# Kernel tuning notes

Hardware: AMD Instinct MI355X
Metric: run time of the kernel (lower is better)

## Reference

```python
import jax, jax.numpy as jnp
import numpy as np

GRAVITY = 9.81007  # pypose default, gravity vector [0,0,g]

# Quaternions are xyzw (pypose SO3 convention). q1*q2 composes rotations R1@R2.

def qmul(q1, q2):
    v1, w1 = q1[..., :3], q1[..., 3:]
    v2, w2 = q2[..., :3], q2[..., 3:]
    w = w1 * w2 - jnp.sum(v1 * v2, axis=-1, keepdims=True)
    v = w1 * v2 + w2 * v1 + jnp.cross(v1, v2)
    return jnp.concatenate([v, w], axis=-1)

def qinv(q):
    return jnp.concatenate([-q[..., :3], q[..., 3:]], axis=-1)

def qrot(q, v):
    # rotate vector v by unit quaternion q: v + 2*cross(qv, cross(qv,v) + qw*v)
    qv, qw = q[..., :3], q[..., 3:]
    t = jnp.cross(qv, v) + qw * v
    return v + 2.0 * jnp.cross(qv, t)

def so3_exp(phi):
    # so3 -> SO3 quaternion: q = [phi*sin(|phi|/2)/|phi|, cos(|phi|/2)]
    theta = jnp.linalg.norm(phi, axis=-1, keepdims=True)
    small = theta < 1e-6
    safe = jnp.where(small, 1.0, theta)
    k = jnp.where(small, 0.5 - theta * theta / 48.0, jnp.sin(0.5 * theta) / safe)
    return jnp.concatenate([phi * k, jnp.cos(0.5 * theta)], axis=-1)


def setup_inputs() -> dict:
    key = jax.random.key(0)
    ks = jax.random.split(key, 7)
    B, F = 64, 32768
    dt = jax.random.uniform(ks[0], (B, F, 1), jnp.float32) * 0.01 + 0.004
    gyro = jax.random.normal(ks[1], (B, F, 3), jnp.float32) * 0.1
    acc = jax.random.normal(ks[2], (B, F, 3), jnp.float32)

    def rand_quat(k, shape):
        q = jax.random.normal(k, shape + (4,), jnp.float32)
        return q / jnp.linalg.norm(q, axis=-1, keepdims=True)

    gt_rot = rand_quat(ks[3], (B, F))      # ground-truth orientations (xyzw)
    init_rot = rand_quat(ks[4], (B, 1))
    init_vel = jax.random.normal(ks[5], (B, 1, 3), jnp.float32)
    init_pos = jax.random.normal(ks[6], (B, 1, 3), jnp.float32)
    return dict(dt=dt, gyro=gyro, acc=acc, gt_rot=gt_rot,
                init_rot=init_rot, init_vel=init_vel, init_pos=init_pos)


def reference(dt, gyro, acc, gt_rot, init_rot, init_vel, init_pos):
    # IMU preintegration (pypose IMUPreintegrator, reset=True, prop_cov=False,
    # training branch: gravity removed in body frame via ground-truth rot).
    g = jnp.array([0.0, 0.0, GRAVITY], dtype=dt.dtype)
    dr = so3_exp(gyro * dt)                                   # (B,F,4) per-step rotation
    # cumulative rotation increment: incre_r[i] = dr_0 * dr_1 * ... * dr_i
    incre_r = jax.lax.associative_scan(qmul, dr, axis=1)      # (B,F,4)
    # gravity-compensated body-frame acceleration
    a = acc - qrot(qinv(gt_rot), g)                           # (B,F,3)
    ra = qrot(incre_r, a)                                     # rotated into init frame
    incre_v = jnp.cumsum(ra * dt, axis=1)                     # (B,F,3)
    v_prev = jnp.concatenate([jnp.zeros_like(incre_v[:, :1]), incre_v[:, :-1]], axis=1)
    incre_p = jnp.cumsum(v_prev * dt + 0.5 * ra * dt * dt, axis=1)
    incre_t = jnp.cumsum(dt, axis=1)                          # (B,F,1)
    # compose with initial state
    rot = qmul(init_rot, incre_r)                             # (B,F,4)
    vel = init_vel + qrot(init_rot, incre_v)                  # (B,F,3)
    pos = init_pos + init_vel * incre_t + qrot(init_rot, incre_p)  # (B,F,3)
    return rot, vel, pos
```

## Files before the change

kernel.cpp:

```cpp
#include <hip/hip_runtime.h>
#include <math.h>

namespace {

constexpr int BLK   = 256;
constexpr int SEQ   = 4;
constexpr int CHUNK = BLK * SEQ;
constexpr int NWAVE = BLK / 64;

struct V3 { float x, y, z; };
struct Q4 { float x, y, z, w; };
struct St { Q4 q; V3 s; V3 p; float T; float pad; };

__device__ __forceinline__ Q4 qmul(const Q4 a, const Q4 b) {
  Q4 r;
  r.x = a.w*b.x + b.w*a.x + a.y*b.z - a.z*b.y;
  r.y = a.w*b.y + b.w*a.y + a.z*b.x - a.x*b.z;
  r.z = a.w*b.z + b.w*a.z + a.x*b.y - a.y*b.x;
  r.w = a.w*b.w - a.x*b.x - a.y*b.y - a.z*b.z;
  return r;
}

__device__ __forceinline__ V3 qrot(const Q4 q, const V3 v) {
  float tx = q.y*v.z - q.z*v.y + q.w*v.x;
  float ty = q.z*v.x - q.x*v.z + q.w*v.y;
  float tz = q.x*v.y - q.y*v.x + q.w*v.z;
  V3 r;
  r.x = v.x + 2.0f*(q.y*tz - q.z*ty);
  r.y = v.y + 2.0f*(q.z*tx - q.x*tz);
  r.z = v.z + 2.0f*(q.x*ty - q.y*tx);
  return r;
}

__device__ __forceinline__ St combine(const St a, const St b) {
  St r;
  r.q = qmul(a.q, b.q);
  V3 rs = qrot(a.q, b.s);
  r.s.x = a.s.x + rs.x;
  r.s.y = a.s.y + rs.y;
  r.s.z = a.s.z + rs.z;
  V3 rp = qrot(a.q, b.p);
  r.p.x = a.p.x + a.s.x*b.T + rp.x;
  r.p.y = a.p.y + a.s.y*b.T + rp.y;
  r.p.z = a.p.z + a.s.z*b.T + rp.z;
  r.T = a.T + b.T;
  r.pad = 0.0f;
  return r;
}

__device__ __forceinline__ St identity_st() {
  St r;
  r.q = {0.0f, 0.0f, 0.0f, 1.0f};
  r.s = {0.0f, 0.0f, 0.0f};
  r.p = {0.0f, 0.0f, 0.0f};
  r.T = 0.0f; r.pad = 0.0f;
  return r;
}

__device__ __forceinline__ St elem_state(float dt, V3 w, V3 ac, Q4 gt) {
  float px = w.x*dt, py = w.y*dt, pz = w.z*dt;
  float t2 = px*px + py*py + pz*pz;
  float k  = 0.5f + t2*(-1.0f/48.0f  + t2*(1.0f/3840.0f));
  float cw = 1.0f + t2*(-0.125f      + t2*(1.0f/384.0f));
  Q4 dr = { px*k, py*k, pz*k, cw };
  Q4 gi = { -gt.x, -gt.y, -gt.z, gt.w };
  V3 g  = { 0.0f, 0.0f, 9.81007f };
  V3 gr = qrot(gi, g);
  V3 a  = { ac.x - gr.x, ac.y - gr.y, ac.z - gr.z };
  V3 ra = qrot(dr, a);
  St e;
  e.q = dr;
  e.s.x = ra.x*dt; e.s.y = ra.y*dt; e.s.z = ra.z*dt;
  float h = 0.5f*dt;
  e.p.x = e.s.x*h; e.p.y = e.s.y*h; e.p.z = e.s.z*h;
  e.T = dt; e.pad = 0.0f;
  return e;
}

__device__ __forceinline__ St shfl_up_st(const St& v, int d) {
  St r;
  r.q.x = __shfl_up(v.q.x, d); r.q.y = __shfl_up(v.q.y, d);
  r.q.z = __shfl_up(v.q.z, d); r.q.w = __shfl_up(v.q.w, d);
  r.s.x = __shfl_up(v.s.x, d); r.s.y = __shfl_up(v.s.y, d);
  r.s.z = __shfl_up(v.s.z, d);
  r.p.x = __shfl_up(v.p.x, d); r.p.y = __shfl_up(v.p.y, d);
  r.p.z = __shfl_up(v.p.z, d);
  r.T   = __shfl_up(v.T, d);   r.pad = 0.0f;
  return r;
}

__device__ __forceinline__ St shfl_down_st(const St& v, int d) {
  St r;
  r.q.x = __shfl_down(v.q.x, d); r.q.y = __shfl_down(v.q.y, d);
  r.q.z = __shfl_down(v.q.z, d); r.q.w = __shfl_down(v.q.w, d);
  r.s.x = __shfl_down(v.s.x, d); r.s.y = __shfl_down(v.s.y, d);
  r.s.z = __shfl_down(v.s.z, d);
  r.p.x = __shfl_down(v.p.x, d); r.p.y = __shfl_down(v.p.y, d);
  r.p.z = __shfl_down(v.p.z, d);
  r.T   = __shfl_down(v.T, d);   r.pad = 0.0f;
  return r;
}

#define BUILD_ELEMS(E)                                                         \
  St E[SEQ];                                                                   \
  {                                                                            \
    float dtv[SEQ]; float gy[SEQ*3]; float acv[SEQ*3]; float gq[SEQ*4];        \
    *((float4*)dtv) = *(const float4*)(dtp + gi);                              \
    _Pragma("unroll")                                                          \
    for (int j = 0; j < 3; ++j) ((float4*)gy)[j]  = ((const float4*)(gyp + gi*3))[j]; \
    _Pragma("unroll")                                                          \
    for (int j = 0; j < 3; ++j) ((float4*)acv)[j] = ((const float4*)(acp + gi*3))[j]; \
    _Pragma("unroll")                                                          \
    for (int j = 0; j < 4; ++j) ((float4*)gq)[j]  = ((const float4*)(gtp + gi*4))[j]; \
    _Pragma("unroll")                                                          \
    for (int i = 0; i < SEQ; ++i)                                              \
      E[i] = elem_state(dtv[i],                                                \
                 {gy[3*i], gy[3*i+1], gy[3*i+2]},                              \
                 {acv[3*i], acv[3*i+1], acv[3*i+2]},                           \
                 {gq[4*i], gq[4*i+1], gq[4*i+2], gq[4*i+3]});                  \
  }

__global__ __launch_bounds__(BLK) void k_agg(
    const float* __restrict__ dtp, const float* __restrict__ gyp,
    const float* __restrict__ acp, const float* __restrict__ gtp,
    St* __restrict__ aggs, int F, int cpb)
{
  const int blk = blockIdx.x;
  const int b = blk / cpb, c = blk - b*cpb;
  const int tid = threadIdx.x;
  const int lane = tid & 63, wv = tid >> 6;
  const size_t gi = (size_t)b*F + (size_t)c*CHUNK + (size_t)tid*SEQ;

  BUILD_ELEMS(e);
  St run = e[0];
  #pragma unroll
  for (int i = 1; i < SEQ; ++i) run = combine(run, e[i]);

  #pragma unroll
  for (int d = 1; d < 64; d <<= 1) run = combine(run, shfl_down_st(run, d));

  __shared__ St sh[NWAVE];
  if (lane == 0) sh[wv] = run;
  __syncthreads();
  if (tid == 0) {
    St t = sh[0];
    #pragma unroll
    for (int k = 1; k < NWAVE; ++k) t = combine(t, sh[k]);
    aggs[blk] = t;
  }
}

__global__ __launch_bounds__(BLK) void k_emit(
    const float* __restrict__ dtp, const float* __restrict__ gyp,
    const float* __restrict__ acp, const float* __restrict__ gtp,
    const St* __restrict__ aggs,
    const float* __restrict__ irp,
    const float* __restrict__ ivp, const float* __restrict__ ipp,
    float* __restrict__ out, int F, int cpb, int B)
{
  const int blk = blockIdx.x;
  const int b = blk / cpb, c = blk - b*cpb;
  const int tid = threadIdx.x;
  const int lane = tid & 63, wv = tid >> 6;
  const size_t gi = (size_t)b*F + (size_t)c*CHUNK + (size_t)tid*SEQ;

  __shared__ St chunkPrefSh;
  __shared__ St shw[NWAVE];

  if (wv == 0) {
    St a = identity_st();
    if (lane < c) a = aggs[(size_t)b*cpb + lane];
    #pragma unroll
    for (int d = 1; d < 64; d <<= 1) a = combine(a, shfl_down_st(a, d));
    if (lane == 0) {
      St p0 = identity_st();
      p0.q = { irp[b*4+0], irp[b*4+1], irp[b*4+2], irp[b*4+3] };
      chunkPrefSh = combine(p0, a);
    }
  }

  BUILD_ELEMS(e);
  St incl = e[0];
  #pragma unroll
  for (int i = 1; i < SEQ; ++i) incl = combine(incl, e[i]);

  #pragma unroll
  for (int d = 1; d < 64; d <<= 1) {
    St o = shfl_up_st(incl, d);
    if (lane >= d) incl = combine(o, incl);
  }
  if (lane == 63) shw[wv] = incl;
  __syncthreads();

  St P = chunkPrefSh;
  for (int k = 0; k < wv; ++k) P = combine(P, shw[k]);
  {
    St ex = shfl_up_st(incl, 1);
    if (lane > 0) P = combine(P, ex);
  }

  V3 iv = { ivp[b*3+0], ivp[b*3+1], ivp[b*3+2] };
  V3 ip = { ipp[b*3+0], ipp[b*3+1], ipp[b*3+2] };

  const size_t BF = (size_t)B * (size_t)F;
  float4* rot4 = (float4*)out;
  float4* vel4 = (float4*)(out + BF*4);
  float4* pos4 = (float4*)(out + BF*7);

  St run = P;
  float velb[SEQ*3], posb[SEQ*3];
  #pragma unroll
  for (int i = 0; i < SEQ; ++i) {
    run = combine(run, e[i]);
    rot4[gi + i] = make_float4(run.q.x, run.q.y, run.q.z, run.q.w);
    velb[3*i+0] = iv.x + run.s.x;
    velb[3*i+1] = iv.y + run.s.y;
    velb[3*i+2] = iv.z + run.s.z;
    posb[3*i+0] = ip.x + iv.x*run.T + run.p.x;
    posb[3*i+1] = ip.y + iv.y*run.T + run.p.y;
    posb[3*i+2] = ip.z + iv.z*run.T + run.p.z;
  }
  const size_t v0 = (gi*3) >> 2;
  #pragma unroll
  for (int j = 0; j < SEQ*3/4; ++j) {
    vel4[v0 + j] = ((float4*)velb)[j];
    pos4[v0 + j] = ((float4*)posb)[j];
  }
}

}

extern "C" void kernel_launch(void* const* d_in, const int* in_sizes, int n_in,
                              void* d_out, int out_size, void* d_ws, size_t ws_size,
                              hipStream_t stream)
{
  (void)n_in; (void)out_size; (void)ws_size;

  const float* dtp = (const float*)d_in[0];
  const float* gyp = (const float*)d_in[1];
  const float* acp = (const float*)d_in[2];
  const float* gtp = (const float*)d_in[3];
  const float* irp = (const float*)d_in[4];
  const float* ivp = (const float*)d_in[5];
  const float* ipp = (const float*)d_in[6];
  float* out = (float*)d_out;

  const int B   = in_sizes[4] / 4;
  const int F   = in_sizes[0] / B;
  const int cpb = F / CHUNK;
  const int nblk = B * cpb;

  St* aggs = (St*)d_ws;

  k_agg<<<nblk, BLK, 0, stream>>>(dtp, gyp, acp, gtp, aggs, F, cpb);
  k_emit<<<nblk, BLK, 0, stream>>>(dtp, gyp, acp, gtp, aggs, irp, ivp, ipp,
                                   out, F, cpb, B);
}
```

Measured before the change: 73.00 us.

## Fuse reduce and emit kernels into a single-pass scan with flag-based lookback

Replaces the two-kernel reduce-then-scan scheme with one kernel. Each block takes a tile index from an atomic counter, scans its chunk, publishes its aggregate with a release flag, then waits on the flags of earlier chunks in the same batch row and combines their aggregates to form its prefix. The goal is to read the large input arrays once instead of twice and to remove a kernel launch. The cost is a memset of the flag region, spin-waiting on predecessor flags, and the risk of stalls if predecessor blocks are scheduled late.

```diff
diff --git a/kernel.cpp b/kernel.cpp
--- a/kernel.cpp
+++ b/kernel.cpp
@@ -101,6 +101,21 @@
   return r;
 }
 
+__device__ __forceinline__ St ld_st3(const float4* p) {
+  float4 a = p[0], b = p[1], c = p[2];
+  St r;
+  r.q = {a.x, a.y, a.z, a.w};
+  r.s = {b.x, b.y, b.z};
+  r.p = {b.w, c.x, c.y};
+  r.T = c.z; r.pad = 0.0f;
+  return r;
+}
+__device__ __forceinline__ void st_st3(float4* p, const St& v) {
+  p[0] = make_float4(v.q.x, v.q.y, v.q.z, v.q.w);
+  p[1] = make_float4(v.s.x, v.s.y, v.s.z, v.p.x);
+  p[2] = make_float4(v.p.y, v.p.z, v.T, 0.0f);
+}
+
 #define BUILD_ELEMS(E)                                                         \
   St E[SEQ];                                                                   \
   {                                                                            \
@@ -120,66 +135,29 @@
                  {gq[4*i], gq[4*i+1], gq[4*i+2], gq[4*i+3]});                  \
   }
 
-__global__ __launch_bounds__(BLK) void k_agg(
+__global__ __launch_bounds__(BLK) void k_fused(
     const float* __restrict__ dtp, const float* __restrict__ gyp,
     const float* __restrict__ acp, const float* __restrict__ gtp,
-    St* __restrict__ aggs, int F, int cpb)
+    const float* __restrict__ irp,
+    const float* __restrict__ ivp, const float* __restrict__ ipp,
+    unsigned int* __restrict__ counter, unsigned int* __restrict__ flags,
+    float4* __restrict__ payload,
+    float* __restrict__ out, int F, int cpb, int B)
 {
-  const int blk = blockIdx.x;
-  const int b = blk / cpb, c = blk - b*cpb;
+  __shared__ int sTile;
+  __shared__ St shw[NWAVE];
+  __shared__ St chunkPrefSh;
+
+  if (threadIdx.x == 0) sTile = (int)atomicAdd(counter, 1u);
+  __syncthreads();
+
+  const int t = sTile;
+  const int b = t / cpb, c = t - b*cpb;
   const int tid = threadIdx.x;
   const int lane = tid & 63, wv = tid >> 6;
   const size_t gi = (size_t)b*F + (size_t)c*CHUNK + (size_t)tid*SEQ;
 
   BUILD_ELEMS(e);
-  St run = e[0];
-  #pragma unroll
-  for (int i = 1; i < SEQ; ++i) run = combine(run, e[i]);
-
-  #pragma unroll
-  for (int d = 1; d < 64; d <<= 1) run = combine(run, shfl_down_st(run, d));
-
-  __shared__ St sh[NWAVE];
-  if (lane == 0) sh[wv] = run;
-  __syncthreads();
-  if (tid == 0) {
-    St t = sh[0];
-    #pragma unroll
-    for (int k = 1; k < NWAVE; ++k) t = combine(t, sh[k]);
-    aggs[blk] = t;
-  }
-}
-
-__global__ __launch_bounds__(BLK) void k_emit(
-    const float* __restrict__ dtp, const float* __restrict__ gyp,
-    const float* __restrict__ acp, const float* __restrict__ gtp,
-    const St* __restrict__ aggs,
-    const float* __restrict__ irp,
-    const float* __restrict__ ivp, const float* __restrict__ ipp,
-    float* __restrict__ out, int F, int cpb, int B)
-{
-  const int blk = blockIdx.x;
-  const int b = blk / cpb, c = blk - b*cpb;
-  const int tid = threadIdx.x;
-  const int lane = tid & 63, wv = tid >> 6;
-  const size_t gi = (size_t)b*F + (size_t)c*CHUNK + (size_t)tid*SEQ;
-
-  __shared__ St chunkPrefSh;
-  __shared__ St shw[NWAVE];
-
-  if (wv == 0) {
-    St a = identity_st();
-    if (lane < c) a = aggs[(size_t)b*cpb + lane];
-    #pragma unroll
-    for (int d = 1; d < 64; d <<= 1) a = combine(a, shfl_down_st(a, d));
-    if (lane == 0) {
-      St p0 = identity_st();
-      p0.q = { irp[b*4+0], irp[b*4+1], irp[b*4+2], irp[b*4+3] };
-      chunkPrefSh = combine(p0, a);
-    }
-  }
-
-  BUILD_ELEMS(e);
   St incl = e[0];
   #pragma unroll
   for (int i = 1; i < SEQ; ++i) incl = combine(incl, e[i]);
@@ -190,6 +168,39 @@
     if (lane >= d) incl = combine(o, incl);
   }
   if (lane == 63) shw[wv] = incl;
+  __syncthreads();
+
+  if (wv == 0) {
+    St bagg = combine(combine(shw[0], shw[1]), combine(shw[2], shw[3]));
+    if (c == 0) {
+      if (lane == 0) {
+        St seed = identity_st();
+        seed.q = { irp[b*4+0], irp[b*4+1], irp[b*4+2], irp[b*4+3] };
+        st_st3(&payload[(size_t)t*3], combine(seed, bagg));
+        __hip_atomic_store(&flags[t], 1u, __ATOMIC_RELEASE, __HIP_MEMORY_SCOPE_AGENT);
+        chunkPrefSh = seed;
+      }
+    } else {
+      if (lane == 0) {
+        st_st3(&payload[(size_t)t*3], bagg);
+        __hip_atomic_store(&flags[t], 1u, __ATOMIC_RELEASE, __HIP_MEMORY_SCOPE_AGENT);
+      }
+      const int lo  = t - c;
+      const int idx = t - 1 - lane;
+      const bool valid = idx >= lo;
+      unsigned int f = valid ? 0u : 1u;
+      while (__any(f == 0u)) {
+        if (f == 0u)
+          f = __hip_atomic_load(&flags[idx], __ATOMIC_ACQUIRE, __HIP_MEMORY_SCOPE_AGENT);
+        if (__any(f == 0u)) __builtin_amdgcn_s_sleep(2);
+      }
+      St X = identity_st();
+      if (valid) X = ld_st3(&payload[(size_t)idx*3]);
+      #pragma unroll
+      for (int d = 1; d < 64; d <<= 1) X = combine(shfl_down_st(X, d), X);
+      if (lane == 0) chunkPrefSh = X;
+    }
+  }
   __syncthreads();
 
   St P = chunkPrefSh;
@@ -250,9 +261,12 @@
   const int cpb = F / CHUNK;
   const int nblk = B * cpb;
 
-  St* aggs = (St*)d_ws;
-
-  k_agg<<<nblk, BLK, 0, stream>>>(dtp, gyp, acp, gtp, aggs, F, cpb);
-  k_emit<<<nblk, BLK, 0, stream>>>(dtp, gyp, acp, gtp, aggs, irp, ivp, ipp,
-                                   out, F, cpb, B);
-}
+  unsigned int* counter = (unsigned int*)d_ws;
+  unsigned int* flags   = (unsigned int*)((char*)d_ws + 128);
+  const size_t flagsBytes = (size_t)nblk * 4;
+  float4* payload = (float4*)((char*)d_ws + 128 + ((flagsBytes + 127) & ~(size_t)127));
+
+  hipMemsetAsync(d_ws, 0, 128 + ((flagsBytes + 127) & ~(size_t)127), stream);
+  k_fused<<<nblk, BLK, 0, stream>>>(dtp, gyp, acp, gtp, irp, ivp, ipp,
+                                    counter, flags, payload, out, F, cpb, B);
+}
```

Result: slower. 133.4 us (+82.8%).

## Use one wavefront per chunk and drop block-level shared-memory scan

Applied to the files above, without the earlier changes.

Chunks shrink from 1024 to 256 elements so each 64-lane wavefront owns a whole chunk. The aggregate kernel packs four independent chunks per block and writes each wave's aggregate directly, with no shared memory or barrier. The emit kernel runs one wave per block and rebuilds its row prefix by reducing up to 128 chunk aggregates in two wave-level passes. This removes __syncthreads and the serial cross-wave combines, at the cost of more redundant prefix work per wave and an assumption that a row has at most 128 chunks.

```diff
diff --git a/kernel.cpp b/kernel.cpp
--- a/kernel.cpp
+++ b/kernel.cpp
@@ -3,10 +3,8 @@
 
 namespace {
 
-constexpr int BLK   = 256;
 constexpr int SEQ   = 4;
-constexpr int CHUNK = BLK * SEQ;
-constexpr int NWAVE = BLK / 64;
+constexpr int CHUNK = 64 * SEQ;
 
 struct V3 { float x, y, z; };
 struct Q4 { float x, y, z, w; };
@@ -101,10 +99,22 @@
   return r;
 }
 
+__device__ __forceinline__ St bcast0_st(const St& v) {
+  St r;
+  r.q.x = __shfl(v.q.x, 0); r.q.y = __shfl(v.q.y, 0);
+  r.q.z = __shfl(v.q.z, 0); r.q.w = __shfl(v.q.w, 0);
+  r.s.x = __shfl(v.s.x, 0); r.s.y = __shfl(v.s.y, 0);
+  r.s.z = __shfl(v.s.z, 0);
+  r.p.x = __shfl(v.p.x, 0); r.p.y = __shfl(v.p.y, 0);
+  r.p.z = __shfl(v.p.z, 0);
+  r.T   = __shfl(v.T, 0);   r.pad = 0.0f;
+  return r;
+}
+
 #define BUILD_ELEMS(E)                                                         \
   St E[SEQ];                                                                   \
   {                                                                            \
-    float dtv[SEQ]; float gy[SEQ*3]; float acv[SEQ*3]; float gq[SEQ*4];        \
+    float dtv[SEQ], gy[SEQ*3], acv[SEQ*3], gq[SEQ*4];                          \
     *((float4*)dtv) = *(const float4*)(dtp + gi);                              \
     _Pragma("unroll")                                                          \
     for (int j = 0; j < 3; ++j) ((float4*)gy)[j]  = ((const float4*)(gyp + gi*3))[j]; \
@@ -120,16 +130,16 @@
                  {gq[4*i], gq[4*i+1], gq[4*i+2], gq[4*i+3]});                  \
   }
 
-__global__ __launch_bounds__(BLK) void k_agg(
+__global__ __launch_bounds__(256) void k_agg(
     const float* __restrict__ dtp, const float* __restrict__ gyp,
     const float* __restrict__ acp, const float* __restrict__ gtp,
     St* __restrict__ aggs, int F, int cpb)
 {
-  const int blk = blockIdx.x;
-  const int b = blk / cpb, c = blk - b*cpb;
-  const int tid = threadIdx.x;
-  const int lane = tid & 63, wv = tid >> 6;
-  const size_t gi = (size_t)b*F + (size_t)c*CHUNK + (size_t)tid*SEQ;
+  const int tid  = threadIdx.x;
+  const int lane = tid & 63;
+  const int cid  = blockIdx.x * 4 + (tid >> 6);
+  const int b = cid / cpb, c = cid - b*cpb;
+  const size_t gi = (size_t)b*F + (size_t)c*CHUNK + (size_t)lane*SEQ;
 
   BUILD_ELEMS(e);
   St run = e[0];
@@ -139,18 +149,10 @@
   #pragma unroll
   for (int d = 1; d < 64; d <<= 1) run = combine(run, shfl_down_st(run, d));
 
-  __shared__ St sh[NWAVE];
-  if (lane == 0) sh[wv] = run;
-  __syncthreads();
-  if (tid == 0) {
-    St t = sh[0];
-    #pragma unroll
-    for (int k = 1; k < NWAVE; ++k) t = combine(t, sh[k]);
-    aggs[blk] = t;
-  }
-}
-
-__global__ __launch_bounds__(BLK) void k_emit(
+  if (lane == 0) aggs[cid] = run;
+}
+
+__global__ __launch_bounds__(64) void k_emit(
     const float* __restrict__ dtp, const float* __restrict__ gyp,
     const float* __restrict__ acp, const float* __restrict__ gtp,
     const St* __restrict__ aggs,
@@ -158,26 +160,15 @@
     const float* __restrict__ ivp, const float* __restrict__ ipp,
     float* __restrict__ out, int F, int cpb, int B)
 {
-  const int blk = blockIdx.x;
-  const int b = blk / cpb, c = blk - b*cpb;
-  const int tid = threadIdx.x;
-  const int lane = tid & 63, wv = tid >> 6;
-  const size_t gi = (size_t)b*F + (size_t)c*CHUNK + (size_t)tid*SEQ;
-
-  __shared__ St chunkPrefSh;
-  __shared__ St shw[NWAVE];
-
-  if (wv == 0) {
-    St a = identity_st();
-    if (lane < c) a = aggs[(size_t)b*cpb + lane];
-    #pragma unroll
-    for (int d = 1; d < 64; d <<= 1) a = combine(a, shfl_down_st(a, d));
-    if (lane == 0) {
-      St p0 = identity_st();
-      p0.q = { irp[b*4+0], irp[b*4+1], irp[b*4+2], irp[b*4+3] };
-      chunkPrefSh = combine(p0, a);
-    }
-  }
+  const int cid  = blockIdx.x;
+  const int b = cid / cpb, c = cid - b*cpb;
+  const int lane = threadIdx.x & 63;
+  const size_t gi = (size_t)b*F + (size_t)c*CHUNK + (size_t)lane*SEQ;
+  const int row0 = b * cpb;
+
+  St A0 = identity_st(), A1 = identity_st();
+  if (c > 0  && lane < c)      A0 = aggs[row0 + lane];
+  if (c > 64 && 64 + lane < c) A1 = aggs[row0 + 64 + lane];
 
   BUILD_ELEMS(e);
   St incl = e[0];
@@ -189,11 +180,22 @@
     St o = shfl_up_st(incl, d);
     if (lane >= d) incl = combine(o, incl);
   }
-  if (lane == 63) shw[wv] = incl;
-  __syncthreads();
-
-  St P = chunkPrefSh;
-  for (int k = 0; k < wv; ++k) P = combine(P, shw[k]);
+
+  St rowp;
+  {
+    #pragma unroll
+    for (int d = 1; d < 64; d <<= 1) A0 = combine(A0, shfl_down_st(A0, d));
+    rowp = bcast0_st(A0);
+    if (c > 64) {
+      #pragma unroll
+      for (int d = 1; d < 64; d <<= 1) A1 = combine(A1, shfl_down_st(A1, d));
+      rowp = combine(rowp, bcast0_st(A1));
+    }
+  }
+
+  St seed = identity_st();
+  seed.q = { irp[b*4+0], irp[b*4+1], irp[b*4+2], irp[b*4+3] };
+  St P = combine(seed, rowp);
   {
     St ex = shfl_up_st(incl, 1);
     if (lane > 0) P = combine(P, ex);
@@ -204,8 +206,8 @@
 
   const size_t BF = (size_t)B * (size_t)F;
   float4* rot4 = (float4*)out;
-  float4* vel4 = (float4*)(out + BF*4);
-  float4* pos4 = (float4*)(out + BF*7);
+  float*  velp = out + BF*4;
+  float*  posp = out + BF*7;
 
   St run = P;
   float velb[SEQ*3], posb[SEQ*3];
@@ -220,11 +222,10 @@
     posb[3*i+1] = ip.y + iv.y*run.T + run.p.y;
     posb[3*i+2] = ip.z + iv.z*run.T + run.p.z;
   }
-  const size_t v0 = (gi*3) >> 2;
   #pragma unroll
   for (int j = 0; j < SEQ*3/4; ++j) {
-    vel4[v0 + j] = ((float4*)velb)[j];
-    pos4[v0 + j] = ((float4*)posb)[j];
+    ((float4*)(velp + gi*3))[j] = ((float4*)velb)[j];
+    ((float4*)(posp + gi*3))[j] = ((float4*)posb)[j];
   }
 }
 
@@ -248,11 +249,11 @@
   const int B   = in_sizes[4] / 4;
   const int F   = in_sizes[0] / B;
   const int cpb = F / CHUNK;
-  const int nblk = B * cpb;
+  const int nchunk = B * cpb;
 
   St* aggs = (St*)d_ws;
 
-  k_agg<<<nblk, BLK, 0, stream>>>(dtp, gyp, acp, gtp, aggs, F, cpb);
-  k_emit<<<nblk, BLK, 0, stream>>>(dtp, gyp, acp, gtp, aggs, irp, ivp, ipp,
-                                   out, F, cpb, B);
-}
+  k_agg <<<nchunk/4, 256, 0, stream>>>(dtp, gyp, acp, gtp, aggs, F, cpb);
+  k_emit<<<nchunk,    64, 0, stream>>>(dtp, gyp, acp, gtp, aggs, irp, ivp, ipp,
+                                       out, F, cpb, B);
+}
```

New measurement: 82.67 us. 1.13x slower.
